# Performance work log

Hardware: AMD Instinct MI355X
Metric: run time of the kernel (lower is better)

Reference implementation:

```python
import jax, jax.numpy as jnp
import numpy as np
from itertools import combinations

SEQ_LEN = 8
FEAT = 2048
SET_SIZE = 2
DOUT = 1152
WAY = 5
SHOT = 5
NQ = 500
MAX_LEN = int(SEQ_LEN * 1.5)
LN_EPS = 1e-5

TUPLES = np.array(list(combinations(range(SEQ_LEN), SET_SIZE)), dtype=np.int32)  # [T, SET_SIZE]
T_LEN = TUPLES.shape[0]  # C(8,2) = 28

def _positional_encoding(d_model, max_len):
    pos = np.arange(max_len, dtype=np.float32)[:, None]
    div = np.exp(np.arange(0, d_model, 2, dtype=np.float32) * (-np.log(10000.0) / d_model))
    pe = np.zeros((max_len, d_model), dtype=np.float32)
    pe[:, 0::2] = np.sin(pos * div)
    pe[:, 1::2] = np.cos(pos * div)
    return jnp.asarray(pe)

PE = _positional_encoding(FEAT, MAX_LEN)  # dropout is identity in eval mode

def _layernorm(x, gamma, beta):
    mu = jnp.mean(x, axis=-1, keepdims=True)
    var = jnp.var(x, axis=-1, keepdims=True)
    return (x - mu) * jax.lax.rsqrt(var + LN_EPS) * gamma + beta

def setup_inputs() -> dict:
    key = jax.random.key(0)
    ks = jax.random.split(key, 8)
    din = FEAT * SET_SIZE
    sc = 1.0 / np.sqrt(din)
    return {
        "support_set": jax.random.normal(ks[0], (WAY * SHOT, SEQ_LEN, FEAT), jnp.float32),
        "support_labels": jnp.repeat(jnp.arange(WAY, dtype=jnp.int32), SHOT),  # sorted, balanced episode
        "queries": jax.random.normal(ks[1], (NQ, SEQ_LEN, FEAT), jnp.float32),
        "k_w": jax.random.normal(ks[2], (din, DOUT), jnp.float32) * sc,
        "k_b": jnp.zeros((DOUT,), jnp.float32),
        "v_w": jax.random.normal(ks[3], (din, DOUT), jnp.float32) * sc,
        "v_b": jnp.zeros((DOUT,), jnp.float32),
        "ln_k_gamma": jnp.ones((DOUT,), jnp.float32),
        "ln_k_beta": jnp.zeros((DOUT,), jnp.float32),
        "global_temperature": jnp.asarray(1.0, jnp.float32),
        "temperature_weight": jnp.ones((1,), jnp.float32),
    }

def reference(support_set, support_labels, queries, k_w, k_b, v_w, v_b,
              ln_k_gamma, ln_k_beta, global_temperature, temperature_weight):
    n_q = queries.shape[0]
    # positional encoding (dropout is eval-mode identity)
    s = support_set + PE[:SEQ_LEN]
    q = queries + PE[:SEQ_LEN]
    # gather frame tuples: [n, T, SET_SIZE, FEAT] -> [n, T, SET_SIZE*FEAT]
    s_t = s[:, TUPLES, :].reshape(WAY * SHOT, T_LEN, SET_SIZE * FEAT)
    q_t = q[:, TUPLES, :].reshape(n_q, T_LEN, SET_SIZE * FEAT)
    # K / V projections; LayerNorm only on K (as in the module)
    s_ks = _layernorm(s_t @ k_w + k_b, ln_k_gamma, ln_k_beta)
    q_ks = _layernorm(q_t @ k_w + k_b, ln_k_gamma, ln_k_beta)
    s_vs = s_t @ v_w + v_b
    q_vs = q_t @ v_w + v_b
    # labels are sorted & balanced -> per-class slices are a reshape
    class_k = s_ks.reshape(WAY, SHOT, T_LEN, DOUT)
    class_v = s_vs.reshape(WAY, SHOT, T_LEN, DOUT)
    # scores[c,q,t,k,u] = <q_ks[q,t], class_k[c,k,u]> / sqrt(DOUT)
    scores = jnp.einsum('qtd,ckud->cqtku', q_ks, class_k) / np.sqrt(DOUT)
    # softmax jointly over (support-clip k, support-tuple u) per query tuple t
    attn = jax.nn.softmax(scores.reshape(WAY, n_q, T_LEN, SHOT * T_LEN), axis=-1)
    attn = attn.reshape(WAY, n_q, T_LEN, SHOT, T_LEN)
    # prototype = sum over support clips of attn @ class_v
    proto = jnp.einsum('cqtku,ckud->cqtd', attn, class_v)  # [WAY, NQ, T, DOUT]
    diff = q_vs[None] - proto
    dist = jnp.sum(diff * diff, axis=(-2, -1)) / T_LEN  # [WAY, NQ]
    logits = (-dist * global_temperature * temperature_weight[0]).T  # [NQ, WAY]
    return logits
```

## Files before the change

kernel.cpp:

```cpp
#include <hip/hip_runtime.h>

typedef __bf16 bf16;
typedef __attribute__((ext_vector_type(8))) __bf16 bf16x8;
typedef __attribute__((ext_vector_type(4))) float f32x4;

#define AS1 __attribute__((address_space(1)))
#define AS3 __attribute__((address_space(3)))

__device__ __constant__ int c_T0[28] = {0,0,0,0,0,0,0,1,1,1,1,1,1,2,2,2,2,2,3,3,3,3,4,4,4,5,5,6};
__device__ __constant__ int c_T1[28] = {1,2,3,4,5,6,7,2,3,4,5,6,7,3,4,5,6,7,4,5,6,7,5,6,7,6,7,7};

__global__ __launch_bounds__(256) void fill_pack(
    const float* __restrict__ queries, const float* __restrict__ support,
    const float* __restrict__ kw, const float* __restrict__ vw,
    bf16* __restrict__ X, bf16* __restrict__ Wp)
{
    __shared__ float t[32][33];
    const int tid = threadIdx.x;
    if (blockIdx.x < 4224) {
        const int f = blockIdx.x;
        bf16* row = X + (long)f * 2048;
        const int d0 = tid << 3;
        if (f >= 4200) {
            bf16x8 z;
            #pragma unroll
            for (int i = 0; i < 8; ++i) z[i] = (bf16)0.f;
            *(bf16x8*)(row + d0) = z;
            return;
        }
        const float* src = (f < 4000) ? (queries + (long)f * 2048)
                                      : (support + (long)(f - 4000) * 2048);
        const int s = f & 7;
        bf16x8 o;
        #pragma unroll
        for (int i = 0; i < 8; ++i) {
            int d = d0 + i;
            float dv = __expf((float)(d >> 1) * -0.008994473019508f);
            float ang = (float)s * dv;
            float pe = (d & 1) ? __cosf(ang) : __sinf(ang);
            o[i] = (bf16)(src[d] + pe);
        }
        *(bf16x8*)(row + d0) = o;
    } else {
        const int b = blockIdx.x - 4224;
        const int k0 = (b & 63) << 5, n0g = (b >> 6) << 5;
        const int tx = tid & 31, ty = tid >> 5;
        const int j = n0g / 1152, nc = n0g % 1152;
        const float* src = ((j < 2) ? kw : vw) + (long)(((j & 1) << 11) + k0) * 1152 + nc;
        #pragma unroll
        for (int i = 0; i < 4; ++i)
            t[ty + (i << 3)][tx] = src[(long)(ty + (i << 3)) * 1152 + tx];
        __syncthreads();
        #pragma unroll
        for (int i = 0; i < 4; ++i)
            Wp[(long)(n0g + ty + (i << 3)) * 2048 + k0 + tx] = (bf16)t[tx][ty + (i << 3)];
    }
}

template <typename OutT>
__global__ __launch_bounds__(256) void gemm_bt(
    const bf16* __restrict__ A, long lda, const bf16* __restrict__ B, long ldb,
    OutT* __restrict__ C, int N, int K, float scale, int tiles_n)
{
    __shared__ __align__(16) bf16 lA[128 * 32];
    __shared__ __align__(16) bf16 lB[128 * 32];
    const int tid = threadIdx.x;
    const int wid = tid >> 6, lane = tid & 63;
    const int wm = (wid >> 1) << 6, wn = (wid & 1) << 6;
    const int quad = lane >> 4, l16 = lane & 15;
    const int tm = blockIdx.x / tiles_n, tn = blockIdx.x % tiles_n;
    const int m0 = tm << 7, n0 = tn << 7;
    const bf16* Abase = A + (long)m0 * lda;

    f32x4 acc[4][4];
    #pragma unroll
    for (int i = 0; i < 4; ++i)
        #pragma unroll
        for (int j = 0; j < 4; ++j)
            #pragma unroll
            for (int r = 0; r < 4; ++r) acc[i][j][r] = 0.f;

    const int srow = lane >> 2, scol = (lane & 3) << 3;
    for (int kk = 0; kk < K; kk += 32) {
        __syncthreads();
        #pragma unroll
        for (int p = 0; p < 2; ++p) {
            const int rbase = (wid << 5) + (p << 4);
            const bf16* ga = Abase + (long)(rbase + srow) * lda + kk + scol;
            const bf16* gb = B + (long)(n0 + rbase + srow) * ldb + kk + scol;
            __builtin_amdgcn_global_load_lds((const AS1 unsigned int*)ga,
                                             (AS3 unsigned int*)(lA + rbase * 32), 16, 0, 0);
            __builtin_amdgcn_global_load_lds((const AS1 unsigned int*)gb,
                                             (AS3 unsigned int*)(lB + rbase * 32), 16, 0, 0);
        }
        __builtin_amdgcn_s_waitcnt(0);
        __syncthreads();
        bf16x8 af[4], bfr[4];
        #pragma unroll
        for (int i = 0; i < 4; ++i)
            af[i] = *(const bf16x8*)(lA + (wm + (i << 4) + l16) * 32 + (quad << 3));
        #pragma unroll
        for (int j = 0; j < 4; ++j)
            bfr[j] = *(const bf16x8*)(lB + (wn + (j << 4) + l16) * 32 + (quad << 3));
        #pragma unroll
        for (int i = 0; i < 4; ++i)
            #pragma unroll
            for (int j = 0; j < 4; ++j)
                acc[i][j] = __builtin_amdgcn_mfma_f32_16x16x32_bf16(af[i], bfr[j], acc[i][j], 0, 0, 0);
    }
    #pragma unroll
    for (int i = 0; i < 4; ++i) {
        const int row = m0 + wm + (i << 4) + (quad << 2);
        #pragma unroll
        for (int j = 0; j < 4; ++j) {
            const int col = n0 + wn + (j << 4) + l16;
            OutT* cp = C + (long)row * N + col;
            #pragma unroll
            for (int r = 0; r < 4; ++r) cp[(long)r * N] = (OutT)(acc[i][j][r] * scale);
        }
    }
}

__global__ __launch_bounds__(256) void gemm_frames(
    const bf16* __restrict__ H, const bf16* __restrict__ Bk,
    const bf16* __restrict__ svs, bf16* __restrict__ FG, bf16* __restrict__ G5)
{
    __shared__ __align__(16) bf16 lA[128 * 32];
    __shared__ __align__(16) bf16 lB[128 * 32];
    const int tid = threadIdx.x;
    const int wid = tid >> 6, lane = tid & 63;
    const int wm = (wid >> 1) << 6, wn = (wid & 1) << 6;
    const int quad = lane >> 4, l16 = lane & 15;
    const bool gram = (int)blockIdx.x >= 792;
    int seg = 4, tm, tn;
    const bf16* Abase;
    long la;
    const bf16* B;
    if (!gram) {
        seg = blockIdx.x / 198;
        int r = blockIdx.x % 198;
        tm = r / 6; tn = r % 6;
        Abase = H + seg * 1152 + (long)(tm << 7) * 4608;
        la = 4608;
        B = (seg < 2) ? Bk : svs;
    } else {
        int r = blockIdx.x - 792;
        tm = r / 6; tn = r % 6;
        Abase = svs + (long)(tm << 7) * 1152;
        la = 1152;
        B = svs;
    }
    const int n0 = tn << 7;

    f32x4 acc[4][4];
    #pragma unroll
    for (int i = 0; i < 4; ++i)
        #pragma unroll
        for (int j = 0; j < 4; ++j)
            #pragma unroll
            for (int r = 0; r < 4; ++r) acc[i][j][r] = 0.f;

    const int srow = lane >> 2, scol = (lane & 3) << 3;
    for (int kk = 0; kk < 1152; kk += 32) {
        __syncthreads();
        #pragma unroll
        for (int p = 0; p < 2; ++p) {
            const int rbase = (wid << 5) + (p << 4);
            const bf16* ga = Abase + (long)(rbase + srow) * la + kk + scol;
            const bf16* gb = B + (long)(n0 + rbase + srow) * 1152 + kk + scol;
            __builtin_amdgcn_global_load_lds((const AS1 unsigned int*)ga,
                                             (AS3 unsigned int*)(lA + rbase * 32), 16, 0, 0);
            __builtin_amdgcn_global_load_lds((const AS1 unsigned int*)gb,
                                             (AS3 unsigned int*)(lB + rbase * 32), 16, 0, 0);
        }
        __builtin_amdgcn_s_waitcnt(0);
        __syncthreads();
        bf16x8 af[4], bfr[4];
        #pragma unroll
        for (int i = 0; i < 4; ++i)
            af[i] = *(const bf16x8*)(lA + (wm + (i << 4) + l16) * 32 + (quad << 3));
        #pragma unroll
        for (int j = 0; j < 4; ++j)
            bfr[j] = *(const bf16x8*)(lB + (wn + (j << 4) + l16) * 32 + (quad << 3));
        #pragma unroll
        for (int i = 0; i < 4; ++i)
            #pragma unroll
            for (int j = 0; j < 4; ++j)
                acc[i][j] = __builtin_amdgcn_mfma_f32_16x16x32_bf16(af[i], bfr[j], acc[i][j], 0, 0, 0);
    }
    #pragma unroll
    for (int i = 0; i < 4; ++i) {
        const int rloc = (tm << 7) + wm + (i << 4) + (quad << 2);
        #pragma unroll
        for (int j = 0; j < 4; ++j) {
            const int col = n0 + wn + (j << 4) + l16;
            #pragma unroll
            for (int r = 0; r < 4; ++r) {
                const int row = rloc + r;
                if (!gram) {
                    FG[(long)(seg * 4224 + row) * 768 + col] = (bf16)acc[i][j][r];
                } else {
                    if (row < 700 && col < 700 && row / 140 == col / 140) {
                        int cc = row / 140;
                        G5[((long)cc * 144 + (row - cc * 140)) * 160 + (col - cc * 140)]
                            = (bf16)acc[i][j][r];
                    }
                }
            }
        }
    }
}

__global__ __launch_bounds__(256) void support_stats(
    const bf16* __restrict__ H, const float* __restrict__ kb,
    const float* __restrict__ vb, const float* __restrict__ gamma,
    const float* __restrict__ beta,
    bf16* __restrict__ Bk, bf16* __restrict__ svs,
    float* __restrict__ gd, float* __restrict__ kbd,
    float* __restrict__ bd2, float* __restrict__ bdot,
    float* __restrict__ MU, float* __restrict__ RS, float* __restrict__ QS)
{
    __shared__ __align__(16) char smem[2 * 9216 * 2 + 512];
    const int tid = threadIdx.x;
    const int wid = tid >> 6, lane = tid & 63;
    if ((int)blockIdx.x < 768) {
        const int u = blockIdx.x;
        bf16* outK = Bk + (long)u * 1152;
        bf16* outV = svs + (long)u * 1152;
        if (u >= 700) {
            for (int d = tid; d < 1152; d += 256) { outK[d] = (bf16)0.f; outV[d] = (bf16)0.f; }
            if (tid == 0) { gd[u] = 0.f; kbd[u] = 0.f; bd2[u] = 0.f; bdot[u] = 0.f; }
            return;
        }
        float* s1 = (float*)smem;
        float* s2 = s1 + 4;
        float* sr = s2 + 4;
        const int n = u / 28, t = u - n * 28;
        const int fi = 4000 + (n << 3) + c_T0[t];
        const int fj = 4000 + (n << 3) + c_T1[t];
        const bf16* Hi = H + (long)fi * 4608;
        const bf16* Hj = H + (long)fj * 4608;
        float xv[5];
        float sum = 0.f, sumsq = 0.f;
        #pragma unroll
        for (int it = 0; it < 5; ++it) {
            int d = tid + (it << 8);
            float x = 0.f;
            if (d < 1152) {
                x = (float)Hi[d] + (float)Hj[1152 + d] + kb[d];
                sum += x; sumsq += x * x;
            }
            xv[it] = x;
        }
        #pragma unroll
        for (int off = 32; off > 0; off >>= 1) {
            sum += __shfl_xor(sum, off, 64);
            sumsq += __shfl_xor(sumsq, off, 64);
        }
        if ((tid & 63) == 0) { s1[wid] = sum; s2[wid] = sumsq; }
        __syncthreads();
        sum = s1[0] + s1[1] + s1[2] + s1[3];
        sumsq = s2[0] + s2[1] + s2[2] + s2[3];
        const float mu = sum * (1.f / 1152.f);
        const float var = sumsq * (1.f / 1152.f) - mu * mu;
        const float rs = rsqrtf(var + 1e-5f);
        float g_ = 0.f, k_ = 0.f, b_ = 0.f, v_ = 0.f;
        #pragma unroll
        for (int it = 0; it < 5; ++it) {
            int d = tid + (it << 8);
            if (d < 1152) {
                float gm = gamma[d];
                float sk = (xv[it] - mu) * rs * gm + beta[d];
                outK[d] = (bf16)(gm * sk);
                g_ += gm * sk;
                k_ += kb[d] * gm * sk;
                b_ += beta[d] * sk;
                float sv = (float)Hi[2304 + d] + (float)Hj[3456 + d] + vb[d];
                outV[d] = (bf16)sv;
                v_ += vb[d] * sv;
            }
        }
        #pragma unroll
        for (int off = 32; off > 0; off >>= 1) {
            g_ += __shfl_xor(g_, off, 64);
            k_ += __shfl_xor(k_, off, 64);
            b_ += __shfl_xor(b_, off, 64);
            v_ += __shfl_xor(v_, off, 64);
        }
        if ((tid & 63) == 0) { sr[wid * 4 + 0] = g_; sr[wid * 4 + 1] = k_; sr[wid * 4 + 2] = b_; sr[wid * 4 + 3] = v_; }
        __syncthreads();
        if (tid == 0) {
            gd[u]   = sr[0] + sr[4] + sr[8]  + sr[12];
            kbd[u]  = sr[1] + sr[5] + sr[9]  + sr[13];
            bd2[u]  = sr[2] + sr[6] + sr[10] + sr[14];
            bdot[u] = sr[3] + sr[7] + sr[11] + sr[15];
        }
        return;
    }
    const int s_ = blockIdx.x - 768;
    const bool kside = s_ < 500;
    const int q = kside ? s_ : s_ - 500;
    const int co = kside ? 0 : 2304;
    const float* bias = kside ? kb : vb;
    bf16* Ft = (bf16*)smem;
    bf16* Fb = Ft + 9216;
    float* fl = (float*)(smem + 36864);
    float* Sa = fl;
    float* Qa = fl + 8;
    float* Ca = fl + 16;
    float* Sb_ = fl + 24;
    float* Qb_ = fl + 32;
    float* Cb_ = fl + 40;
    float* Pp = fl + 48;
    float* Sk2 = fl + 76;
    for (int idx = tid; idx < 1152; idx += 256) {
        int row = idx / 144, col = (idx - row * 144) << 3;
        const bf16* src = H + (long)((q << 3) + row) * 4608 + co;
        *(bf16x8*)(Ft + row * 1152 + col) = *(const bf16x8*)(src + col);
        *(bf16x8*)(Fb + row * 1152 + col) = *(const bf16x8*)(src + 1152 + col);
    }
    __syncthreads();
    for (int task = wid; task < 45; task += 4) {
        float s0 = 0.f, s1v = 0.f, s2v = 0.f;
        if (task < 16) {
            const bf16* p = (task < 8) ? (Ft + task * 1152) : (Fb + (task - 8) * 1152);
            for (int c = lane << 3; c < 1152; c += 512) {
                bf16x8 v = *(const bf16x8*)(p + c);
                #pragma unroll
                for (int k = 0; k < 8; ++k) {
                    float f = (float)v[k];
                    s0 += f; s1v += f * f; s2v += f * bias[c + k];
                }
            }
        } else if (task < 44) {
            int t = task - 16;
            const bf16* pa = Ft + c_T0[t] * 1152;
            const bf16* pb = Fb + c_T1[t] * 1152;
            for (int c = lane << 3; c < 1152; c += 512) {
                bf16x8 a = *(const bf16x8*)(pa + c);
                bf16x8 b = *(const bf16x8*)(pb + c);
                #pragma unroll
                for (int k = 0; k < 8; ++k) s0 += (float)a[k] * (float)b[k];
            }
        } else {
            for (int c = lane << 3; c < 1152; c += 512) {
                #pragma unroll
                for (int k = 0; k < 8; ++k) { float f = bias[c + k]; s0 += f; s1v += f * f; }
            }
        }
        #pragma unroll
        for (int off = 32; off > 0; off >>= 1) {
            s0 += __shfl_xor(s0, off, 64);
            s1v += __shfl_xor(s1v, off, 64);
            s2v += __shfl_xor(s2v, off, 64);
        }
        if (lane == 0) {
            if (task < 8)       { Sa[task] = s0; Qa[task] = s1v; Ca[task] = s2v; }
            else if (task < 16) { Sb_[task - 8] = s0; Qb_[task - 8] = s1v; Cb_[task - 8] = s2v; }
            else if (task < 44) Pp[task - 16] = s0;
            else                { Sk2[0] = s0; Sk2[1] = s1v; }
        }
    }
    __syncthreads();
    if (kside) {
        if (tid < 28) {
            int i = c_T0[tid], j = c_T1[tid];
            float mu = (Sa[i] + Sb_[j] + Sk2[0]) * (1.f / 1152.f);
            float ex2 = (Qa[i] + Qb_[j] + Sk2[1] + 2.f * (Pp[tid] + Ca[i] + Cb_[j])) * (1.f / 1152.f);
            float var = ex2 - mu * mu;
            int m = q * 28 + tid;
            MU[m] = mu;
            RS[m] = rsqrtf(var + 1e-5f);
        }
    } else {
        if (tid < 64) {
            float term = 0.f;
            if (lane < 28) {
                int i = c_T0[lane], j = c_T1[lane];
                term = Qa[i] + Qb_[j] + Sk2[1] + 2.f * (Pp[lane] + Ca[i] + Cb_[j]);
            }
            #pragma unroll
            for (int off = 32; off > 0; off >>= 1) term += __shfl_xor(term, off, 64);
            if (lane == 0) QS[q] = term;
        }
    }
}

__global__ __launch_bounds__(320) void assemble_softmax(
    const bf16* __restrict__ Fkt, const bf16* __restrict__ Fkb,
    const float* __restrict__ MU, const float* __restrict__ RS,
    const float* __restrict__ gd, const float* __restrict__ kbd,
    const float* __restrict__ bd2, bf16* __restrict__ attn5)
{
    const int m = blockIdx.x, tid = threadIdx.x;
    if (m >= 14000) {
        #pragma unroll
        for (int c = 0; c < 5; ++c)
            for (int d = tid; d < 144; d += 320)
                attn5[((long)c * 14080 + m) * 144 + d] = (bf16)0.f;
        return;
    }
    const int q = m / 28, t = m - q * 28;
    const bf16* ft = Fkt + (long)((q << 3) + c_T0[t]) * 768;
    const bf16* fb = Fkb + (long)((q << 3) + c_T1[t]) * 768;
    const float mu = MU[m], rs = RS[m];
    const int w = tid >> 6, lane = tid & 63;
    const int base = w * 140;
    const float sc = 0.029462782549439484f;
    int u0 = base + lane, u1 = base + 64 + lane, u2 = base + 128 + lane;
    float v0 = (rs * ((float)ft[u0] + (float)fb[u0] + kbd[u0] - mu * gd[u0]) + bd2[u0]) * sc;
    float v1 = (rs * ((float)ft[u1] + (float)fb[u1] + kbd[u1] - mu * gd[u1]) + bd2[u1]) * sc;
    float v2 = (lane < 12)
             ? (rs * ((float)ft[u2] + (float)fb[u2] + kbd[u2] - mu * gd[u2]) + bd2[u2]) * sc
             : -1e30f;
    float mx = fmaxf(fmaxf(v0, v1), v2);
    #pragma unroll
    for (int off = 32; off > 0; off >>= 1) mx = fmaxf(mx, __shfl_xor(mx, off, 64));
    float e0 = __expf(v0 - mx), e1 = __expf(v1 - mx);
    float e2 = (lane < 12) ? __expf(v2 - mx) : 0.f;
    float s = e0 + e1 + e2;
    #pragma unroll
    for (int off = 32; off > 0; off >>= 1) s += __shfl_xor(s, off, 64);
    const float inv = 1.f / s;
    bf16* aw = attn5 + ((long)w * 14080 + m) * 144;
    aw[lane] = (bf16)(e0 * inv);
    aw[64 + lane] = (bf16)(e1 * inv);
    if (lane < 12) aw[128 + lane] = (bf16)(e2 * inv);
    else if (lane < 16) aw[128 + lane] = (bf16)0.f;
}

__global__ __launch_bounds__(256) void class_dist(
    const bf16* __restrict__ attn5, const bf16* __restrict__ G5,
    const bf16* __restrict__ FG, const float* __restrict__ bdot,
    float* __restrict__ dist)
{
    __shared__ __align__(16) bf16 lA[128 * 168];
    __shared__ __align__(16) bf16 lG[144 * 168];
    const int tid = threadIdx.x;
    const int c = blockIdx.x / 110, tm = blockIdx.x % 110;
    const long m0 = (long)tm * 128;
    const bf16* Abase = attn5 + ((long)c * 14080 + m0) * 144;
    for (int v = tid; v < 128 * 18; v += 256) {
        int r = v / 18, k = (v - r * 18) << 3;
        *(bf16x8*)(lA + r * 168 + k) = *(const bf16x8*)(Abase + (long)r * 144 + k);
    }
    {
        int r = tid >> 1, k = 144 + ((tid & 1) << 3);
        bf16x8 z;
        #pragma unroll
        for (int i = 0; i < 8; ++i) z[i] = (bf16)0.f;
        *(bf16x8*)(lA + r * 168 + k) = z;
    }
    const bf16* Gbase = G5 + (long)c * 144 * 160;
    for (int v = tid; v < 144 * 20; v += 256) {
        int r = v / 20, k = (v - r * 20) << 3;
        *(bf16x8*)(lG + r * 168 + k) = *(const bf16x8*)(Gbase + r * 160 + k);
    }
    __syncthreads();
    const int wid = tid >> 6, lane = tid & 63;
    const int quad = lane >> 4, l16 = lane & 15;
    const int wr = wid << 5;
    f32x4 acc[2][9];
    #pragma unroll
    for (int i = 0; i < 2; ++i)
        #pragma unroll
        for (int j = 0; j < 9; ++j)
            #pragma unroll
            for (int r = 0; r < 4; ++r) acc[i][j][r] = 0.f;
    #pragma unroll
    for (int kk = 0; kk < 160; kk += 32) {
        bf16x8 af0 = *(const bf16x8*)(lA + (wr + l16) * 168 + kk + (quad << 3));
        bf16x8 af1 = *(const bf16x8*)(lA + (wr + 16 + l16) * 168 + kk + (quad << 3));
        #pragma unroll
        for (int j = 0; j < 9; ++j) {
            bf16x8 bf_ = *(const bf16x8*)(lG + ((j << 4) + l16) * 168 + kk + (quad << 3));
            acc[0][j] = __builtin_amdgcn_mfma_f32_16x16x32_bf16(af0, bf_, acc[0][j], 0, 0, 0);
            acc[1][j] = __builtin_amdgcn_mfma_f32_16x16x32_bf16(af1, bf_, acc[1][j], 0, 0, 0);
        }
    }
    #pragma unroll
    for (int i = 0; i < 2; ++i) {
        #pragma unroll
        for (int r = 0; r < 4; ++r) {
            const int rl = wr + (i << 4) + (quad << 2) + r;
            const long m = m0 + rl;
            if (m >= 14000) continue;
            const int q = (int)(m / 28), t = (int)(m - (long)q * 28);
            const int fi = (q << 3) + c_T0[t], fj = (q << 3) + c_T1[t];
            const bf16* ft = FG + (long)(8448 + fi) * 768 + c * 140;
            const bf16* fb = FG + (long)(12672 + fj) * 768 + c * 140;
            const float* bd = bdot + c * 140;
            float s = 0.f;
            #pragma unroll
            for (int j = 0; j < 9; ++j) {
                const int col = (j << 4) + l16;
                float a = (float)lA[rl * 168 + col];
                float wv = (float)ft[col] + (float)fb[col] + bd[col];
                s += a * (acc[i][j][r] - 2.f * wv);
            }
            #pragma unroll
            for (int off = 1; off < 16; off <<= 1) s += __shfl_xor(s, off, 64);
            if (l16 == 0) atomicAdd(&dist[c * 500 + q], s);
        }
    }
}

__global__ void finalize(const float* __restrict__ dist, const float* __restrict__ QS,
                         const float* __restrict__ gt, const float* __restrict__ tw,
                         float* __restrict__ out)
{
    int i = blockIdx.x * 256 + threadIdx.x;
    if (i < 2500) {
        int q = i / 5, c = i - q * 5;
        out[i] = -(dist[c * 500 + q] + QS[q]) * (gt[0] * tw[0] * (1.f / 28.f));
    }
}

extern "C" void kernel_launch(void* const* d_in, const int* in_sizes, int n_in,
                              void* d_out, int out_size, void* d_ws, size_t ws_size,
                              hipStream_t stream)
{
    const float* support = (const float*)d_in[0];
    const float* queries = (const float*)d_in[2];
    const float* kw      = (const float*)d_in[3];
    const float* kb      = (const float*)d_in[4];
    const float* vw      = (const float*)d_in[5];
    const float* vb      = (const float*)d_in[6];
    const float* gamma   = (const float*)d_in[7];
    const float* beta    = (const float*)d_in[8];
    const float* gt      = (const float*)d_in[9];
    const float* tw      = (const float*)d_in[10];
    float* out = (float*)d_out;

    char* ws = (char*)d_ws;
    size_t off = 0;
    auto alloc = [&](size_t b) { char* p = ws + off; off += (b + 255) & ~(size_t)255; return p; };
    bf16* X      = (bf16*)alloc(4224ull * 2048 * 2);
    bf16* Wp     = (bf16*)alloc(4608ull * 2048 * 2);
    bf16* H      = (bf16*)alloc(4224ull * 4608 * 2);
    bf16* FG     = (bf16*)alloc(16896ull * 768 * 2);
    bf16* attn5  = (bf16*)alloc(5ull * 14080 * 144 * 2);
    bf16* Bk     = (bf16*)alloc(768ull * 1152 * 2);
    bf16* svs    = (bf16*)alloc(768ull * 1152 * 2);
    bf16* G5     = (bf16*)alloc(5ull * 144 * 160 * 2);
    float* dist  = (float*)alloc(5 * 500 * 4);
    float* MU    = (float*)alloc(14000ull * 4);
    float* RS    = (float*)alloc(14000ull * 4);
    float* gd    = (float*)alloc(768 * 4);
    float* kbd   = (float*)alloc(768 * 4);
    float* bd2   = (float*)alloc(768 * 4);
    float* bdot  = (float*)alloc(768 * 4);
    float* QS    = (float*)alloc(500 * 4);

    hipMemsetAsync(G5, 0, 5ull * 144 * 160 * 2 + 5 * 500 * 4, stream);
    fill_pack<<<4224 + 9216, 256, 0, stream>>>(queries, support, kw, vw, X, Wp);
    gemm_bt<bf16><<<33 * 36, 256, 0, stream>>>(X, 2048, Wp, 2048, H, 4608, 2048, 1.f, 36);
    support_stats<<<1768, 256, 0, stream>>>(H, kb, vb, gamma, beta, Bk, svs,
                                            gd, kbd, bd2, bdot, MU, RS, QS);
    gemm_frames<<<828, 256, 0, stream>>>(H, Bk, svs, FG, G5);
    assemble_softmax<<<14080, 320, 0, stream>>>(FG, FG + 4224ull * 768, MU, RS, gd, kbd, bd2, attn5);
    class_dist<<<550, 256, 0, stream>>>(attn5, G5, FG, bdot, dist);
    finalize<<<10, 256, 0, stream>>>(dist, QS, gt, tw, out);
}
```

Measured before the change: 399.9 us.

## Fuse softmax assembly into class_dist and trim gemm_frames padded row tiles

Removes the separate assemble_softmax kernel. class_dist now computes the layernormed scores and the softmax for its 128-row tile directly into shared memory instead of reading a precomputed attn5 buffer from global memory. gemm_frames also drops one padded M-tile per segment (33 to 32 tiles, 828 to 804 blocks), relying on row 4096+ tiles being unused. This saves a kernel launch and the global write and read of the attention buffer. In exchange, the softmax work runs serially per wave across 32 rows inside class_dist. Any tile rows beyond 4096 that are no longer produced would have to be truly unused.

Result: slower. 459.3 us (+14.9%).

```diff
diff --git a/kernel.cpp b/kernel.cpp
--- a/kernel.cpp
+++ b/kernel.cpp
@@ -131,20 +131,20 @@
     const int wid = tid >> 6, lane = tid & 63;
     const int wm = (wid >> 1) << 6, wn = (wid & 1) << 6;
     const int quad = lane >> 4, l16 = lane & 15;
-    const bool gram = (int)blockIdx.x >= 792;
+    const bool gram = (int)blockIdx.x >= 768;
     int seg = 4, tm, tn;
     const bf16* Abase;
     long la;
     const bf16* B;
     if (!gram) {
-        seg = blockIdx.x / 198;
-        int r = blockIdx.x % 198;
+        seg = blockIdx.x / 192;
+        int r = blockIdx.x % 192;
         tm = r / 6; tn = r % 6;
         Abase = H + seg * 1152 + (long)(tm << 7) * 4608;
         la = 4608;
         B = (seg < 2) ? Bk : svs;
     } else {
-        int r = blockIdx.x - 792;
+        int r = blockIdx.x - 768;
         tm = r / 6; tn = r % 6;
         Abase = svs + (long)(tm << 7) * 1152;
         la = 1152;
@@ -386,52 +386,11 @@
     }
 }
 
-__global__ __launch_bounds__(320) void assemble_softmax(
-    const bf16* __restrict__ Fkt, const bf16* __restrict__ Fkb,
-    const float* __restrict__ MU, const float* __restrict__ RS,
-    const float* __restrict__ gd, const float* __restrict__ kbd,
-    const float* __restrict__ bd2, bf16* __restrict__ attn5)
-{
-    const int m = blockIdx.x, tid = threadIdx.x;
-    if (m >= 14000) {
-        #pragma unroll
-        for (int c = 0; c < 5; ++c)
-            for (int d = tid; d < 144; d += 320)
-                attn5[((long)c * 14080 + m) * 144 + d] = (bf16)0.f;
-        return;
-    }
-    const int q = m / 28, t = m - q * 28;
-    const bf16* ft = Fkt + (long)((q << 3) + c_T0[t]) * 768;
-    const bf16* fb = Fkb + (long)((q << 3) + c_T1[t]) * 768;
-    const float mu = MU[m], rs = RS[m];
-    const int w = tid >> 6, lane = tid & 63;
-    const int base = w * 140;
-    const float sc = 0.029462782549439484f;
-    int u0 = base + lane, u1 = base + 64 + lane, u2 = base + 128 + lane;
-    float v0 = (rs * ((float)ft[u0] + (float)fb[u0] + kbd[u0] - mu * gd[u0]) + bd2[u0]) * sc;
-    float v1 = (rs * ((float)ft[u1] + (float)fb[u1] + kbd[u1] - mu * gd[u1]) + bd2[u1]) * sc;
-    float v2 = (lane < 12)
-             ? (rs * ((float)ft[u2] + (float)fb[u2] + kbd[u2] - mu * gd[u2]) + bd2[u2]) * sc
-             : -1e30f;
-    float mx = fmaxf(fmaxf(v0, v1), v2);
-    #pragma unroll
-    for (int off = 32; off > 0; off >>= 1) mx = fmaxf(mx, __shfl_xor(mx, off, 64));
-    float e0 = __expf(v0 - mx), e1 = __expf(v1 - mx);
-    float e2 = (lane < 12) ? __expf(v2 - mx) : 0.f;
-    float s = e0 + e1 + e2;
-    #pragma unroll
-    for (int off = 32; off > 0; off >>= 1) s += __shfl_xor(s, off, 64);
-    const float inv = 1.f / s;
-    bf16* aw = attn5 + ((long)w * 14080 + m) * 144;
-    aw[lane] = (bf16)(e0 * inv);
-    aw[64 + lane] = (bf16)(e1 * inv);
-    if (lane < 12) aw[128 + lane] = (bf16)(e2 * inv);
-    else if (lane < 16) aw[128 + lane] = (bf16)0.f;
-}
-
 __global__ __launch_bounds__(256) void class_dist(
-    const bf16* __restrict__ attn5, const bf16* __restrict__ G5,
-    const bf16* __restrict__ FG, const float* __restrict__ bdot,
+    const bf16* __restrict__ FG, const float* __restrict__ MU,
+    const float* __restrict__ RS, const float* __restrict__ gd,
+    const float* __restrict__ kbd, const float* __restrict__ bd2,
+    const bf16* __restrict__ G5, const float* __restrict__ bdot,
     float* __restrict__ dist)
 {
     __shared__ __align__(16) bf16 lA[128 * 168];
@@ -439,25 +398,52 @@
     const int tid = threadIdx.x;
     const int c = blockIdx.x / 110, tm = blockIdx.x % 110;
     const long m0 = (long)tm * 128;
-    const bf16* Abase = attn5 + ((long)c * 14080 + m0) * 144;
-    for (int v = tid; v < 128 * 18; v += 256) {
-        int r = v / 18, k = (v - r * 18) << 3;
-        *(bf16x8*)(lA + r * 168 + k) = *(const bf16x8*)(Abase + (long)r * 144 + k);
-    }
-    {
-        int r = tid >> 1, k = 144 + ((tid & 1) << 3);
-        bf16x8 z;
-        #pragma unroll
-        for (int i = 0; i < 8; ++i) z[i] = (bf16)0.f;
-        *(bf16x8*)(lA + r * 168 + k) = z;
-    }
+    const int wid = tid >> 6, lane = tid & 63;
     const bf16* Gbase = G5 + (long)c * 144 * 160;
     for (int v = tid; v < 144 * 20; v += 256) {
         int r = v / 20, k = (v - r * 20) << 3;
         *(bf16x8*)(lG + r * 168 + k) = *(const bf16x8*)(Gbase + r * 160 + k);
     }
+    const int cb = c * 140;
+    const float sc = 0.029462782549439484f;
+    for (int i = 0; i < 32; ++i) {
+        const int rl = (wid << 5) + i;
+        const long m = m0 + rl;
+        bf16* aw = lA + rl * 168;
+        if (m >= 14000) {
+            if (lane < 20) {
+                bf16x8 z;
+                #pragma unroll
+                for (int k = 0; k < 8; ++k) z[k] = (bf16)0.f;
+                *(bf16x8*)(aw + (lane << 3)) = z;
+            }
+            continue;
+        }
+        const int q = (int)(m / 28), t = (int)(m - (long)q * 28);
+        const bf16* ft = FG + (long)((q << 3) + c_T0[t]) * 768 + cb;
+        const bf16* fb = FG + ((long)4224 + (q << 3) + c_T1[t]) * 768 + cb;
+        const float mu = MU[m], rs = RS[m];
+        const int u0 = cb + lane, u1 = cb + 64 + lane, u2 = cb + 128 + lane;
+        float v0 = (rs * ((float)ft[lane] + (float)fb[lane] + kbd[u0] - mu * gd[u0]) + bd2[u0]) * sc;
+        float v1 = (rs * ((float)ft[64 + lane] + (float)fb[64 + lane] + kbd[u1] - mu * gd[u1]) + bd2[u1]) * sc;
+        float v2 = (lane < 12)
+                 ? (rs * ((float)ft[128 + lane] + (float)fb[128 + lane] + kbd[u2] - mu * gd[u2]) + bd2[u2]) * sc
+                 : -1e30f;
+        float mx = fmaxf(fmaxf(v0, v1), v2);
+        #pragma unroll
+        for (int off = 32; off > 0; off >>= 1) mx = fmaxf(mx, __shfl_xor(mx, off, 64));
+        float e0 = __expf(v0 - mx), e1 = __expf(v1 - mx);
+        float e2 = (lane < 12) ? __expf(v2 - mx) : 0.f;
+        float s = e0 + e1 + e2;
+        #pragma unroll
+        for (int off = 32; off > 0; off >>= 1) s += __shfl_xor(s, off, 64);
+        const float inv = 1.f / s;
+        aw[lane] = (bf16)(e0 * inv);
+        aw[64 + lane] = (bf16)(e1 * inv);
+        if (lane < 12) aw[128 + lane] = (bf16)(e2 * inv);
+        else if (lane < 32) aw[128 + lane] = (bf16)0.f;
+    }
     __syncthreads();
-    const int wid = tid >> 6, lane = tid & 63;
     const int quad = lane >> 4, l16 = lane & 15;
     const int wr = wid << 5;
     f32x4 acc[2][9];
@@ -487,9 +473,9 @@
             if (m >= 14000) continue;
             const int q = (int)(m / 28), t = (int)(m - (long)q * 28);
             const int fi = (q << 3) + c_T0[t], fj = (q << 3) + c_T1[t];
-            const bf16* ft = FG + (long)(8448 + fi) * 768 + c * 140;
-            const bf16* fb = FG + (long)(12672 + fj) * 768 + c * 140;
-            const float* bd = bdot + c * 140;
+            const bf16* ft = FG + (long)(8448 + fi) * 768 + cb;
+            const bf16* fb = FG + (long)(12672 + fj) * 768 + cb;
+            const float* bd = bdot + cb;
             float s = 0.f;
             #pragma unroll
             for (int j = 0; j < 9; ++j) {
@@ -539,7 +525,6 @@
     bf16* Wp     = (bf16*)alloc(4608ull * 2048 * 2);
     bf16* H      = (bf16*)alloc(4224ull * 4608 * 2);
     bf16* FG     = (bf16*)alloc(16896ull * 768 * 2);
-    bf16* attn5  = (bf16*)alloc(5ull * 14080 * 144 * 2);
     bf16* Bk     = (bf16*)alloc(768ull * 1152 * 2);
     bf16* svs    = (bf16*)alloc(768ull * 1152 * 2);
     bf16* G5     = (bf16*)alloc(5ull * 144 * 160 * 2);
@@ -557,8 +542,7 @@
     gemm_bt<bf16><<<33 * 36, 256, 0, stream>>>(X, 2048, Wp, 2048, H, 4608, 2048, 1.f, 36);
     support_stats<<<1768, 256, 0, stream>>>(H, kb, vb, gamma, beta, Bk, svs,
                                             gd, kbd, bd2, bdot, MU, RS, QS);
-    gemm_frames<<<828, 256, 0, stream>>>(H, Bk, svs, FG, G5);
-    assemble_softmax<<<14080, 320, 0, stream>>>(FG, FG + 4224ull * 768, MU, RS, gd, kbd, bd2, attn5);
-    class_dist<<<550, 256, 0, stream>>>(attn5, G5, FG, bdot, dist);
+    gemm_frames<<<804, 256, 0, stream>>>(H, Bk, svs, FG, G5);
+    class_dist<<<550, 256, 0, stream>>>(FG, MU, RS, gd, kbd, bd2, G5, bdot, dist);
     finalize<<<10, 256, 0, stream>>>(dist, QS, gt, tw, out);
 }
```
